# Kernel tuning notes

Hardware: AMD Instinct MI355X
Metric: run time of the kernel (lower is better)

Reference implementation:

```python
import jax, jax.numpy as jnp
import numpy as np

N, E = 50000, 800000
S, V, RBF_DIM = 128, 16, 16
RBF_DMAX = 20.0
MSG_NORM = 10.0
EPS = 1e-8
DVH_M = V + 1            # message GVP: dim_vectors_in = V + 1 (edge direction appended), dim_h = max(17,16) = 17
FIN_M = S + RBF_DIM      # message GVP scalar input = node scalars + rbf(dist)
DVH_U = 2 * V            # update GVP: dim_vectors_in = 2V (node + aggregated), dim_h = 32
FIN_U = 2 * S


def _rbf(D):
    # [E] -> [E, RBF_DIM], matches torch _rbf with D_min=0, D_max=20, D_count=16
    D_mu = jnp.linspace(0.0, RBF_DMAX, RBF_DIM)
    D_sigma = RBF_DMAX / RBF_DIM
    return jnp.exp(-(((D[:, None] - D_mu[None, :]) / D_sigma) ** 2))


def _gvp(s, v, Wh, Wu, Wf, bf, Wg, bg):
    # s: [n, F_in], v: [n, V_in, 3]; faithful to GVP.forward with sigmoid vector gating
    Vh = jnp.einsum('nvc,vh->nhc', v, Wh)          # [n, H, 3]
    Vu = jnp.einsum('nhc,ho->noc', Vh, Wu)         # [n, V_out, 3]
    sh = jnp.sqrt(jnp.clip(jnp.sum(Vh * Vh, -1), EPS))  # _norm_no_nan
    feats_out = jax.nn.silu(jnp.concatenate([s, sh], -1) @ Wf + bf)
    gate = jax.nn.sigmoid(feats_out @ Wg + bg)[..., None]
    return feats_out, gate * Vu


def _gvp_layernorm(s, v, gamma, beta):
    mu = jnp.mean(s, -1, keepdims=True)
    var = jnp.mean((s - mu) ** 2, -1, keepdims=True)
    s_out = (s - mu) / jnp.sqrt(var + 1e-5) * gamma + beta
    vn = jnp.clip(jnp.sum(v * v, -1, keepdims=True), EPS)        # [N, V, 1]
    vn = jnp.sqrt(jnp.mean(vn, -2, keepdims=True) + 1e-5) + 1e-5  # [N, 1, 1]
    return s_out, v / vn


def setup_inputs() -> dict:
    key = jax.random.key(0)
    ks = jax.random.split(key, 14)
    rn = lambda k, shp, sc: (jax.random.normal(k, shp, dtype=jnp.float32) * sc)
    inp = {
        's': rn(ks[0], (N, S), 1.0),
        'v': rn(ks[1], (N, V, 3), 1.0),
        'x': rn(ks[2], (N, 3), 5.0),
        # message GVP params
        'Wh_m': rn(ks[3], (DVH_M, DVH_M), 1.0 / np.sqrt(DVH_M)),
        'Wu_m': rn(ks[4], (DVH_M, V), 1.0 / np.sqrt(DVH_M)),
        'Wf_m': rn(ks[5], (DVH_M + FIN_M, S), 1.0 / np.sqrt(DVH_M + FIN_M)),
        'bf_m': jnp.zeros((S,), jnp.float32),
        'Wg_m': rn(ks[6], (S, V), 1.0 / np.sqrt(S)),
        'bg_m': jnp.zeros((V,), jnp.float32),
        # update GVP params
        'Wh_u': rn(ks[7], (DVH_U, DVH_U), 1.0 / np.sqrt(DVH_U)),
        'Wu_u': rn(ks[8], (DVH_U, V), 1.0 / np.sqrt(DVH_U)),
        'Wf_u': rn(ks[9], (DVH_U + FIN_U, S), 1.0 / np.sqrt(DVH_U + FIN_U)),
        'bf_u': jnp.zeros((S,), jnp.float32),
        'Wg_u': rn(ks[10], (S, V), 1.0 / np.sqrt(S)),
        'bg_u': jnp.zeros((V,), jnp.float32),
        # layernorm
        'ln_g': jnp.ones((S,), jnp.float32),
        'ln_b': jnp.zeros((S,), jnp.float32),
        'edge_index': jax.random.randint(ks[11], (2, E), 0, N),
    }
    return inp


def reference(s, v, x, Wh_m, Wu_m, Wf_m, bf_m, Wg_m, bg_m,
              Wh_u, Wu_u, Wf_u, bf_u, Wg_u, bg_u, ln_g, ln_b, edge_index):
    src, dst = edge_index[0], edge_index[1]
    # gather + geometric edge features
    dx = x[dst] - x[src]                                   # [E, 3]
    dist = jnp.sqrt(jnp.clip(jnp.sum(dx * dx, -1), EPS))    # [E]
    unit = dx / dist[:, None]
    v_in = jnp.concatenate([v[src], unit[:, None, :]], 1)   # [E, V+1, 3]
    s_in = jnp.concatenate([s[src], _rbf(dist)], -1)        # [E, S+RBF]
    # message GVP
    ms, mv = _gvp(s_in, v_in, Wh_m, Wu_m, Wf_m, bf_m, Wg_m, bg_m)
    # scatter-reduce + message norm
    agg_s = jax.ops.segment_sum(ms, dst, num_segments=N) / MSG_NORM   # [N, S]
    agg_v = jax.ops.segment_sum(mv, dst, num_segments=N) / MSG_NORM   # [N, V, 3]
    # update GVP on concatenated node + aggregated messages
    us, uv = _gvp(jnp.concatenate([s, agg_s], -1), jnp.concatenate([v, agg_v], 1),
                  Wh_u, Wu_u, Wf_u, bf_u, Wg_u, bg_u)
    # residual + GVPLayerNorm
    return _gvp_layernorm(s + us, v + uv, ln_g, ln_b)
```

## Files before the change

### kernel.cpp

```cpp
#include <hip/hip_runtime.h>
#include <hip/hip_bf16.h>
#include <math.h>

#define N_NODES 50000
#define E_EDGES 800000
#define S_DIM 128
#define V_DIM 16
#define HM 17
#define KM 161
#define HU 32
#define KU 288

#define EB 32
#define LDA 164
#define NB 32
#define LDA2 292

__device__ __forceinline__ float bf2f(unsigned short u) {
    union { unsigned int i; float f; } w; w.i = ((unsigned int)u) << 16; return w.f;
}
__device__ __forceinline__ unsigned short f2bf(float f) {
    union { float f; unsigned int i; } w; w.f = f;
    unsigned int x = w.i;
    x += 0x7fff + ((x >> 16) & 1);
    return (unsigned short)(x >> 16);
}
__device__ __forceinline__ float silu_f(float x) { return x / (1.f + __expf(-x)); }
__device__ __forceinline__ float sigm_f(float x) { return 1.f / (1.f + __expf(-x)); }
__device__ __forceinline__ float ldf(const void* p, int i, int m) {
    if (m) return ((const float*)p)[i];
    return bf2f(((const unsigned short*)p)[i]);
}

__global__ void detect_kernel(const unsigned short* __restrict__ s_us,
                              int* __restrict__ flag) {
    int t = threadIdx.x;
    int huge = 0;
    for (int k = 0; k < 16; ++k) {
        unsigned short u = s_us[2 * (t + 64 * k)];
        int e = (u >> 7) & 0xFF;
        if (e > 140) huge = 1;
    }
    if (huge) atomicOr(flag, 1);
}

__global__ void hist_kernel(const int* __restrict__ ei, int* __restrict__ cnt) {
    int i = blockIdx.x * 256 + threadIdx.x;
    if (i < E_EDGES) atomicAdd(&cnt[ei[E_EDGES + i]], 1);
}

__global__ void scan_kernel(int* __restrict__ cnt) {
    __shared__ int buf[1024];
    __shared__ int base_s;
    const int t = threadIdx.x;
    if (t == 0) base_s = 0;
    __syncthreads();
    for (int c0 = 0; c0 < N_NODES; c0 += 1024) {
        int i = c0 + t;
        int v = (i < N_NODES) ? cnt[i] : 0;
        buf[t] = v;
        __syncthreads();
        for (int off = 1; off < 1024; off <<= 1) {
            int tmp = (t >= off) ? buf[t - off] : 0;
            __syncthreads();
            buf[t] += tmp;
            __syncthreads();
        }
        int base = base_s;
        if (i < N_NODES) cnt[i] = base + buf[t] - v;
        __syncthreads();
        if (t == 0) base_s = base + buf[1023];
        __syncthreads();
    }
}

__global__ void scatter_kernel(const int* __restrict__ ei,
                               int* __restrict__ cnt,
                               int* __restrict__ perm) {
    int i = blockIdx.x * 256 + threadIdx.x;
    if (i < E_EDGES) {
        int d = ei[E_EDGES + i];
        int p = atomicAdd(&cnt[d], 1);
        perm[p] = i;
    }
}

__global__ __launch_bounds__(256, 4) void edge_kernel(
    const void* sP, const void* vP, const void* xP,
    const void* WhP, const void* WuP, const void* WfP,
    const void* bfP, const void* WgP, const void* bgP,
    const int* __restrict__ ei,
    const int* __restrict__ perm,
    const int* __restrict__ flagp,
    float* __restrict__ agg_s,
    float* __restrict__ agg_v)
{
    __shared__ float A[EB * LDA];
    __shared__ float Bs[2048];
    __shared__ float WhWu[HM * 16];
    __shared__ float gates[EB * 16];
    __shared__ int srcb[EB], dstb[EB];

    const int t = threadIdx.x;
    const int e0 = blockIdx.x * EB;
    const int m = flagp[0];

    if (t < EB) {
        int eid = perm[e0 + t];
        srcb[t] = ei[eid];
        dstb[t] = ei[E_EDGES + eid];
    }
    if (m) {
        const float* Wh = (const float*)WhP;
        const float* Wu = (const float*)WuP;
        for (int i = t; i < HM * HM; i += 256) gates[i] = Wh[i];
        for (int i = t; i < HM * 16; i += 256) Bs[1664 + i] = Wu[i];
    } else {
        const unsigned short* Wh = (const unsigned short*)WhP;
        const unsigned short* Wu = (const unsigned short*)WuP;
        for (int i = t; i < HM * HM; i += 256) gates[i] = bf2f(Wh[i]);
        for (int i = t; i < HM * 16; i += 256) Bs[1664 + i] = bf2f(Wu[i]);
    }
    __syncthreads();

    for (int idx = t; idx < HM * 16; idx += 256) {
        int vv = idx / 16, o = idx % 16;
        float acc = 0.f;
        for (int h = 0; h < HM; ++h)
            acc += gates[vv * HM + h] * Bs[1664 + h * 16 + o];
        WhWu[idx] = acc;
    }
    {
        int tj = t & 31, te = t >> 5;
        if (m) {
            const float* sF = (const float*)sP;
            for (int r = 0; r < 4; ++r) {
                int e = te + 8 * r;
                float4 u = *(const float4*)(sF + (size_t)srcb[e] * S_DIM + tj * 4);
                float* a = &A[e * LDA + tj * 4];
                a[0] = u.x; a[1] = u.y; a[2] = u.z; a[3] = u.w;
            }
        } else {
            const unsigned short* sU = (const unsigned short*)sP;
            for (int r = 0; r < 4; ++r) {
                int e = te + 8 * r;
                ushort4 u = *(const ushort4*)(sU + (size_t)srcb[e] * S_DIM + tj * 4);
                float* a = &A[e * LDA + tj * 4];
                a[0] = bf2f(u.x); a[1] = bf2f(u.y); a[2] = bf2f(u.z); a[3] = bf2f(u.w);
            }
        }
    }
    if (t < 128) {
        int e = t >> 2, q = t & 3;
        int src = srcb[e];
        float* vin = &Bs[e * 52 + q * 12];
        if (m) {
            const float* vp = (const float*)vP + (size_t)src * 48 + q * 12;
            for (int i = 0; i < 3; ++i) {
                float4 u = *(const float4*)(vp + i * 4);
                vin[i * 4 + 0] = u.x; vin[i * 4 + 1] = u.y;
                vin[i * 4 + 2] = u.z; vin[i * 4 + 3] = u.w;
            }
        } else {
            const unsigned short* vp = (const unsigned short*)vP + (size_t)src * 48 + q * 12;
            for (int i = 0; i < 3; ++i) {
                ushort4 u = *(const ushort4*)(vp + i * 4);
                vin[i * 4 + 0] = bf2f(u.x); vin[i * 4 + 1] = bf2f(u.y);
                vin[i * 4 + 2] = bf2f(u.z); vin[i * 4 + 3] = bf2f(u.w);
            }
        }
        if (q == 0) {
            int dst = dstb[e];
            float dxc[3]; float d2 = 0.f;
            for (int c = 0; c < 3; ++c) {
                float xs = ldf(xP, src * 3 + c, m);
                float xd = ldf(xP, dst * 3 + c, m);
                dxc[c] = xd - xs; d2 += dxc[c] * dxc[c];
            }
            float dist = sqrtf(fmaxf(d2, 1e-8f));
            float inv = 1.f / dist;
            for (int c = 0; c < 3; ++c) Bs[e * 52 + 48 + c] = dxc[c] * inv;
            for (int k = 0; k < 16; ++k) {
                float mu = (20.f / 15.f) * (float)k;
                float z = (dist - mu) * (1.f / 1.25f);
                A[e * LDA + 128 + k] = __expf(-z * z);
            }
        }
    }
    __syncthreads();

    for (int idx = t; idx < EB * HM; idx += 256) {
        int e = idx / HM, h = idx % HM;
        const float* vin = &Bs[e * 52];
        float vh0 = 0.f, vh1 = 0.f, vh2 = 0.f;
        for (int vv = 0; vv < HM; ++vv) {
            float w = gates[vv * HM + h];
            vh0 += vin[vv * 3 + 0] * w;
            vh1 += vin[vv * 3 + 1] * w;
            vh2 += vin[vv * 3 + 2] * w;
        }
        A[e * LDA + 144 + h] = sqrtf(fmaxf(vh0 * vh0 + vh1 * vh1 + vh2 * vh2, 1e-8f));
    }
    float vureg[6];
    for (int r = 0; r < 6; ++r) {
        int idx = t + 256 * r;
        int e = idx / 48, oc = idx % 48, o = oc / 3, c = oc % 3;
        const float* vin = &Bs[e * 52];
        float acc = 0.f;
        for (int vv = 0; vv < HM; ++vv)
            acc += vin[vv * 3 + c] * WhWu[vv * 16 + o];
        vureg[r] = acc;
    }
    __syncthreads();

    const int tj = t & 15, te = t >> 4;
    const int eb = te * 2;
    float acc[2][8];
    #pragma unroll
    for (int i = 0; i < 2; ++i)
        #pragma unroll
        for (int j = 0; j < 8; ++j) acc[i][j] = 0.f;

    for (int kk = 0; kk < KM; kk += 16) {
        int kmax = min(16, KM - kk);
        if (m) {
            const float* WfF = (const float*)WfP;
            for (int idx = t; idx < kmax * 32; idx += 256) {
                int kt = idx >> 5, col4 = (idx & 31) * 4;
                float4 u = *(const float4*)(WfF + (size_t)(kk + kt) * 128 + col4);
                float* b = &Bs[kt * 128 + col4];
                b[0] = u.x; b[1] = u.y; b[2] = u.z; b[3] = u.w;
            }
        } else {
            const unsigned short* WfU = (const unsigned short*)WfP;
            for (int idx = t; idx < kmax * 32; idx += 256) {
                int kt = idx >> 5, col4 = (idx & 31) * 4;
                ushort4 u = *(const ushort4*)(WfU + (size_t)(kk + kt) * 128 + col4);
                float* b = &Bs[kt * 128 + col4];
                b[0] = bf2f(u.x); b[1] = bf2f(u.y); b[2] = bf2f(u.z); b[3] = bf2f(u.w);
            }
        }
        __syncthreads();
        for (int kt = 0; kt < kmax; ++kt) {
            float a0 = A[(eb + 0) * LDA + kk + kt];
            float a1 = A[(eb + 1) * LDA + kk + kt];
            const float* brow = &Bs[kt * 128 + tj];
            #pragma unroll
            for (int jj = 0; jj < 8; ++jj) {
                float b = brow[16 * jj];
                acc[0][jj] += a0 * b; acc[1][jj] += a1 * b;
            }
        }
        __syncthreads();
    }
    float breg[8];
    #pragma unroll
    for (int jj = 0; jj < 8; ++jj) breg[jj] = ldf(bfP, tj + 16 * jj, m);
    #pragma unroll
    for (int i = 0; i < 2; ++i) {
        float* aout = &A[(eb + i) * LDA];
        #pragma unroll
        for (int jj = 0; jj < 8; ++jj)
            aout[tj + 16 * jj] = silu_f(acc[i][jj] + breg[jj]);
    }
    __syncthreads();
    if (m) {
        const float* Wg = (const float*)WgP;
        for (int i = t; i < 2048; i += 256) Bs[i] = Wg[i];
    } else {
        const unsigned short* Wg = (const unsigned short*)WgP;
        for (int i = t; i < 2048; i += 256) Bs[i] = bf2f(Wg[i]);
    }
    __syncthreads();
    for (int r = 0; r < 2; ++r) {
        int idx = t + 256 * r;
        int e = idx / 16, o = idx % 16;
        const float* fe = &A[e * LDA];
        float g = ldf(bgP, o, m);
        for (int j = 0; j < S_DIM; ++j)
            g += fe[j] * Bs[j * 16 + o];
        gates[idx] = sigm_f(g);
    }
    __syncthreads();
    for (int r = 0; r < 6; ++r) {
        int idx = t + 256 * r;
        int e = idx / 48, oc = idx % 48, o = oc / 3;
        (void)oc;
        Bs[idx] = vureg[r] * gates[e * 16 + o];
    }
    __syncthreads();
    if (t < 176) {
        float run = 0.f;
        int cur = dstb[0];
        if (t < 128) {
            const int col = t;
            for (int e = 0; e < EB; ++e) {
                int d = dstb[e];
                if (d != cur) {
                    atomicAdd(&agg_s[(size_t)cur * S_DIM + col], run);
                    run = 0.f; cur = d;
                }
                run += A[e * LDA + col];
            }
            atomicAdd(&agg_s[(size_t)cur * S_DIM + col], run);
        } else {
            const int oc = t - 128;
            for (int e = 0; e < EB; ++e) {
                int d = dstb[e];
                if (d != cur) {
                    atomicAdd(&agg_v[(size_t)cur * 48 + oc], run);
                    run = 0.f; cur = d;
                }
                run += Bs[e * 48 + oc];
            }
            atomicAdd(&agg_v[(size_t)cur * 48 + oc], run);
        }
    }
}

__global__ __launch_bounds__(256) void node_kernel(
    const void* sP, const void* vP,
    const void* WhP, const void* WuP, const void* WfP,
    const void* bfP, const void* WgP, const void* bgP,
    const void* lngP, const void* lnbP,
    const int* __restrict__ flagp,
    const float* __restrict__ agg_s,
    const float* __restrict__ agg_v,
    void* outP)
{
    __shared__ float A2[NB * LDA2];
    __shared__ float Bs2[4096];
    __shared__ float WhWu2[HU * 16];
    __shared__ float gates2[NB * 16];
    __shared__ float WhS[HU * HU];
    __shared__ float mu_s[NB], rstd_s[NB], vn_s[NB];

    const int t = threadIdx.x;
    const int n0 = blockIdx.x * NB;
    const int m = flagp[0];

    if (m) {
        const float* Wh = (const float*)WhP;
        const float* Wu = (const float*)WuP;
        for (int i = t; i < HU * HU; i += 256) WhS[i] = Wh[i];
        for (int i = t; i < HU * 16; i += 256) gates2[i] = Wu[i];
    } else {
        const unsigned short* Wh = (const unsigned short*)WhP;
        const unsigned short* Wu = (const unsigned short*)WuP;
        for (int i = t; i < HU * HU; i += 256) WhS[i] = bf2f(Wh[i]);
        for (int i = t; i < HU * 16; i += 256) gates2[i] = bf2f(Wu[i]);
    }
    if (m) {
        const float* sF = (const float*)sP;
        for (int idx = t; idx < NB * 32; idx += 256) {
            int ni = idx >> 5, col4 = (idx & 31) * 4;
            int n = n0 + ni;
            float* a = &A2[ni * LDA2 + col4];
            if (n < N_NODES) {
                float4 u = *(const float4*)(sF + (size_t)n * 128 + col4);
                a[0] = u.x; a[1] = u.y; a[2] = u.z; a[3] = u.w;
            } else { a[0] = a[1] = a[2] = a[3] = 0.f; }
        }
    } else {
        const unsigned short* sU = (const unsigned short*)sP;
        for (int idx = t; idx < NB * 32; idx += 256) {
            int ni = idx >> 5, col4 = (idx & 31) * 4;
            int n = n0 + ni;
            float* a = &A2[ni * LDA2 + col4];
            if (n < N_NODES) {
                ushort4 u = *(const ushort4*)(sU + (size_t)n * 128 + col4);
                a[0] = bf2f(u.x); a[1] = bf2f(u.y); a[2] = bf2f(u.z); a[3] = bf2f(u.w);
            } else { a[0] = a[1] = a[2] = a[3] = 0.f; }
        }
    }
    for (int idx = t; idx < NB * 32; idx += 256) {
        int ni = idx >> 5, col4 = (idx & 31) * 4;
        int n = n0 + ni;
        float* a = &A2[ni * LDA2 + 128 + col4];
        if (n < N_NODES) {
            float4 u = *(const float4*)(agg_s + (size_t)n * 128 + col4);
            a[0] = u.x * 0.1f; a[1] = u.y * 0.1f; a[2] = u.z * 0.1f; a[3] = u.w * 0.1f;
        } else { a[0] = a[1] = a[2] = a[3] = 0.f; }
    }
    for (int idx = t; idx < NB * 96; idx += 256) {
        int ni = idx / 96, vc = idx % 96;
        int n = n0 + ni;
        float val = 0.f;
        if (n < N_NODES)
            val = (vc < 48) ? ldf(vP, n * 48 + vc, m)
                            : agg_v[(size_t)n * 48 + (vc - 48)] * 0.1f;
        Bs2[ni * 100 + vc] = val;
    }
    __syncthreads();
    for (int idx = t; idx < HU * 16; idx += 256) {
        int vv = idx / 16, o = idx % 16;
        float acc = 0.f;
        for (int h = 0; h < HU; ++h)
            acc += WhS[vv * HU + h] * gates2[h * 16 + o];
        WhWu2[idx] = acc;
    }
    for (int idx = t; idx < NB * HU; idx += 256) {
        int ni = idx / HU, h = idx % HU;
        const float* vc = &Bs2[ni * 100];
        float vh0 = 0.f, vh1 = 0.f, vh2 = 0.f;
        for (int vv = 0; vv < HU; ++vv) {
            float w = WhS[vv * HU + h];
            vh0 += vc[vv * 3 + 0] * w; vh1 += vc[vv * 3 + 1] * w; vh2 += vc[vv * 3 + 2] * w;
        }
        A2[ni * LDA2 + 256 + h] = sqrtf(fmaxf(vh0 * vh0 + vh1 * vh1 + vh2 * vh2, 1e-8f));
    }
    __syncthreads();
    float vureg[6];
    for (int r = 0; r < 6; ++r) {
        int idx = t + 256 * r;
        int ni = idx / 48, oc = idx % 48, o = oc / 3, c = oc % 3;
        const float* vc = &Bs2[ni * 100];
        float acc = 0.f;
        for (int vv = 0; vv < HU; ++vv)
            acc += vc[vv * 3 + c] * WhWu2[vv * 16 + o];
        vureg[r] = acc;
    }
    __syncthreads();

    const int tj = t & 15, tn = t >> 4;
    const int nb = tn * 2;
    float acc[2][8];
    #pragma unroll
    for (int i = 0; i < 2; ++i)
        #pragma unroll
        for (int j = 0; j < 8; ++j) acc[i][j] = 0.f;

    for (int kk = 0; kk < KU; kk += 32) {
        if (m) {
            const float* WfF = (const float*)WfP;
            for (int idx = t; idx < 32 * 32; idx += 256) {
                int kt = idx >> 5, col4 = (idx & 31) * 4;
                float4 u = *(const float4*)(WfF + (size_t)(kk + kt) * 128 + col4);
                float* b = &Bs2[kt * 128 + col4];
                b[0] = u.x; b[1] = u.y; b[2] = u.z; b[3] = u.w;
            }
        } else {
            const unsigned short* WfU = (const unsigned short*)WfP;
            for (int idx = t; idx < 32 * 32; idx += 256) {
                int kt = idx >> 5, col4 = (idx & 31) * 4;
                ushort4 u = *(const ushort4*)(WfU + (size_t)(kk + kt) * 128 + col4);
                float* b = &Bs2[kt * 128 + col4];
                b[0] = bf2f(u.x); b[1] = bf2f(u.y); b[2] = bf2f(u.z); b[3] = bf2f(u.w);
            }
        }
        __syncthreads();
        for (int kt = 0; kt < 32; ++kt) {
            float a0 = A2[(nb + 0) * LDA2 + kk + kt];
            float a1 = A2[(nb + 1) * LDA2 + kk + kt];
            const float* brow = &Bs2[kt * 128 + tj];
            #pragma unroll
            for (int jj = 0; jj < 8; ++jj) {
                float b = brow[16 * jj];
                acc[0][jj] += a0 * b; acc[1][jj] += a1 * b;
            }
        }
        __syncthreads();
    }
    float breg[8];
    #pragma unroll
    for (int jj = 0; jj < 8; ++jj) breg[jj] = ldf(bfP, tj + 16 * jj, m);
    #pragma unroll
    for (int i = 0; i < 2; ++i) {
        float* aout = &A2[(nb + i) * LDA2 + 128];
        #pragma unroll
        for (int jj = 0; jj < 8; ++jj)
            aout[tj + 16 * jj] = silu_f(acc[i][jj] + breg[jj]);
    }
    __syncthreads();
    if (m) {
        const float* Wg = (const float*)WgP;
        for (int i = t; i < 2048; i += 256) Bs2[i] = Wg[i];
    } else {
        const unsigned short* Wg = (const unsigned short*)WgP;
        for (int i = t; i < 2048; i += 256) Bs2[i] = bf2f(Wg[i]);
    }
    __syncthreads();
    for (int r = 0; r < 2; ++r) {
        int idx = t + 256 * r;
        int ni = idx / 16, o = idx % 16;
        const float* fe = &A2[ni * LDA2 + 128];
        float g = ldf(bgP, o, m);
        for (int j = 0; j < 128; ++j)
            g += fe[j] * Bs2[j * 16 + o];
        gates2[idx] = sigm_f(g);
    }
    __syncthreads();
    for (int r = 0; r < 6; ++r) {
        int idx = t + 256 * r;
        int ni = idx / 48, oc = idx % 48, o = oc / 3;
        int n = n0 + ni;
        float vres = 0.f;
        if (n < N_NODES)
            vres = ldf(vP, n * 48 + oc, m) + vureg[r] * gates2[ni * 16 + o];
        Bs2[ni * 48 + oc] = vres;
    }
    __syncthreads();
    if (t < NB) {
        const float* arow = &A2[t * LDA2];
        float sum = 0.f, sumsq = 0.f;
        for (int j = 0; j < 128; ++j) {
            float xr = arow[j] + arow[128 + j];
            sum += xr; sumsq += xr * xr;
        }
        float mu = sum * (1.f / 128.f);
        float var = sumsq * (1.f / 128.f) - mu * mu;
        mu_s[t] = mu;
        rstd_s[t] = rsqrtf(fmaxf(var, 0.f) + 1e-5f);
        const float* vr = &Bs2[t * 48];
        float accv = 0.f;
        for (int o = 0; o < 16; ++o) {
            float mm = vr[o*3]*vr[o*3] + vr[o*3+1]*vr[o*3+1] + vr[o*3+2]*vr[o*3+2];
            accv += fmaxf(mm, 1e-8f);
        }
        vn_s[t] = sqrtf(accv * (1.f / 16.f) + 1e-5f) + 1e-5f;
    }
    __syncthreads();
    float* outF = (float*)outP;
    unsigned short* outU = (unsigned short*)outP;
    for (int idx = t; idx < NB * 128; idx += 256) {
        int ni = idx >> 7, j = idx & 127;
        int n = n0 + ni;
        if (n < N_NODES) {
            float xr = A2[ni * LDA2 + j] + A2[ni * LDA2 + 128 + j];
            float o = (xr - mu_s[ni]) * rstd_s[ni] * ldf(lngP, j, m) + ldf(lnbP, j, m);
            if (m) outF[(size_t)n * 128 + j] = o;
            else   outU[(size_t)n * 128 + j] = f2bf(o);
        }
    }
    for (int idx = t; idx < NB * 48; idx += 256) {
        int ni = idx / 48, oc = idx % 48;
        int n = n0 + ni;
        if (n < N_NODES) {
            float o = Bs2[ni * 48 + oc] / vn_s[ni];
            if (m) outF[(size_t)N_NODES * 128 + (size_t)n * 48 + oc] = o;
            else   outU[(size_t)N_NODES * 128 + (size_t)n * 48 + oc] = f2bf(o);
        }
    }
}

extern "C" void kernel_launch(void* const* d_in, const int* in_sizes, int n_in,
                              void* d_out, int out_size, void* d_ws, size_t ws_size,
                              hipStream_t stream) {
    const int* ei = (const int*)d_in[17];

    int* flag = (int*)d_ws;
    int* cnt = (int*)((char*)d_ws + 64);
    float* agg_s = (float*)((char*)d_ws + 64 + 200000);
    float* agg_v = agg_s + (size_t)N_NODES * 128;
    int* perm = (int*)(agg_v + (size_t)N_NODES * 48);

    hipMemsetAsync(d_ws, 0,
                   64 + 200000 + (size_t)N_NODES * (128 + 48) * sizeof(float),
                   stream);

    detect_kernel<<<1, 64, 0, stream>>>((const unsigned short*)d_in[0], flag);

    hist_kernel<<<(E_EDGES + 255) / 256, 256, 0, stream>>>(ei, cnt);
    scan_kernel<<<1, 1024, 0, stream>>>(cnt);
    scatter_kernel<<<(E_EDGES + 255) / 256, 256, 0, stream>>>(ei, cnt, perm);

    edge_kernel<<<E_EDGES / EB, 256, 0, stream>>>(
        d_in[0], d_in[1], d_in[2], d_in[3], d_in[4], d_in[5],
        d_in[6], d_in[7], d_in[8], ei, perm, flag, agg_s, agg_v);
    node_kernel<<<(N_NODES + NB - 1) / NB, 256, 0, stream>>>(
        d_in[0], d_in[1], d_in[9], d_in[10], d_in[11], d_in[12],
        d_in[13], d_in[14], d_in[15], d_in[16], flag,
        agg_s, agg_v, d_out);
}
```

Before: 2.534 ms.

## Make edge kernel persistent over tiles with Wf and Wg cached in LDS

Each edge block now processes eight 32-edge tiles. In the bf16 path it loads the whole Wf and Wg weights into shared memory once, as bf16, instead of restaging Wf through LDS in chunks for every tile. The scatter pass now writes sorted src/dst arrays directly, which removes the indirection through perm. The trade-offs are more LDS use (launch bounds drop to 2 blocks per CU), fewer blocks, and an fp32 path that reads Wg straight from global memory.

```diff
diff --git a/kernel.cpp b/kernel.cpp
--- a/kernel.cpp
+++ b/kernel.cpp
@@ -12,6 +12,7 @@
 #define KU 288
 
 #define EB 32
+#define TILES 8
 #define LDA 164
 #define NB 32
 #define LDA2 292
@@ -76,50 +77,55 @@
 
 __global__ void scatter_kernel(const int* __restrict__ ei,
                                int* __restrict__ cnt,
-                               int* __restrict__ perm) {
+                               int* __restrict__ src_sorted,
+                               int* __restrict__ dst_sorted) {
     int i = blockIdx.x * 256 + threadIdx.x;
     if (i < E_EDGES) {
         int d = ei[E_EDGES + i];
         int p = atomicAdd(&cnt[d], 1);
-        perm[p] = i;
-    }
-}
-
-__global__ __launch_bounds__(256, 4) void edge_kernel(
+        src_sorted[p] = ei[i];
+        dst_sorted[p] = d;
+    }
+}
+
+__global__ __launch_bounds__(256, 2) void edge_kernel(
     const void* sP, const void* vP, const void* xP,
     const void* WhP, const void* WuP, const void* WfP,
     const void* bfP, const void* WgP, const void* bgP,
-    const int* __restrict__ ei,
-    const int* __restrict__ perm,
+    const int* __restrict__ src_sorted,
+    const int* __restrict__ dst_sorted,
     const int* __restrict__ flagp,
     float* __restrict__ agg_s,
     float* __restrict__ agg_v)
 {
+    __shared__ __align__(16) unsigned short WfU[KM * 128];
+    __shared__ __align__(16) unsigned short WgU[128 * 16];
     __shared__ float A[EB * LDA];
     __shared__ float Bs[2048];
+    __shared__ float WhS[HM * HM];
     __shared__ float WhWu[HM * 16];
     __shared__ float gates[EB * 16];
     __shared__ int srcb[EB], dstb[EB];
 
     const int t = threadIdx.x;
-    const int e0 = blockIdx.x * EB;
     const int m = flagp[0];
 
-    if (t < EB) {
-        int eid = perm[e0 + t];
-        srcb[t] = ei[eid];
-        dstb[t] = ei[E_EDGES + eid];
-    }
     if (m) {
         const float* Wh = (const float*)WhP;
         const float* Wu = (const float*)WuP;
-        for (int i = t; i < HM * HM; i += 256) gates[i] = Wh[i];
+        for (int i = t; i < HM * HM; i += 256) WhS[i] = Wh[i];
         for (int i = t; i < HM * 16; i += 256) Bs[1664 + i] = Wu[i];
     } else {
         const unsigned short* Wh = (const unsigned short*)WhP;
         const unsigned short* Wu = (const unsigned short*)WuP;
-        for (int i = t; i < HM * HM; i += 256) gates[i] = bf2f(Wh[i]);
+        for (int i = t; i < HM * HM; i += 256) WhS[i] = bf2f(Wh[i]);
         for (int i = t; i < HM * 16; i += 256) Bs[1664 + i] = bf2f(Wu[i]);
+        const ushort4* Wf4 = (const ushort4*)WfP;
+        ushort4* WfD = (ushort4*)WfU;
+        for (int i = t; i < (KM * 128) / 4; i += 256) WfD[i] = Wf4[i];
+        const ushort4* Wg4 = (const ushort4*)WgP;
+        ushort4* WgD = (ushort4*)WgU;
+        for (int i = t; i < (128 * 16) / 4; i += 256) WgD[i] = Wg4[i];
     }
     __syncthreads();
 
@@ -127,194 +133,217 @@
         int vv = idx / 16, o = idx % 16;
         float acc = 0.f;
         for (int h = 0; h < HM; ++h)
-            acc += gates[vv * HM + h] * Bs[1664 + h * 16 + o];
+            acc += WhS[vv * HM + h] * Bs[1664 + h * 16 + o];
         WhWu[idx] = acc;
     }
-    {
-        int tj = t & 31, te = t >> 5;
-        if (m) {
-            const float* sF = (const float*)sP;
-            for (int r = 0; r < 4; ++r) {
-                int e = te + 8 * r;
-                float4 u = *(const float4*)(sF + (size_t)srcb[e] * S_DIM + tj * 4);
-                float* a = &A[e * LDA + tj * 4];
-                a[0] = u.x; a[1] = u.y; a[2] = u.z; a[3] = u.w;
-            }
-        } else {
-            const unsigned short* sU = (const unsigned short*)sP;
-            for (int r = 0; r < 4; ++r) {
-                int e = te + 8 * r;
-                ushort4 u = *(const ushort4*)(sU + (size_t)srcb[e] * S_DIM + tj * 4);
-                float* a = &A[e * LDA + tj * 4];
-                a[0] = bf2f(u.x); a[1] = bf2f(u.y); a[2] = bf2f(u.z); a[3] = bf2f(u.w);
-            }
-        }
-    }
-    if (t < 128) {
-        int e = t >> 2, q = t & 3;
-        int src = srcb[e];
-        float* vin = &Bs[e * 52 + q * 12];
-        if (m) {
-            const float* vp = (const float*)vP + (size_t)src * 48 + q * 12;
-            for (int i = 0; i < 3; ++i) {
-                float4 u = *(const float4*)(vp + i * 4);
-                vin[i * 4 + 0] = u.x; vin[i * 4 + 1] = u.y;
-                vin[i * 4 + 2] = u.z; vin[i * 4 + 3] = u.w;
-            }
-        } else {
-            const unsigned short* vp = (const unsigned short*)vP + (size_t)src * 48 + q * 12;
-            for (int i = 0; i < 3; ++i) {
-                ushort4 u = *(const ushort4*)(vp + i * 4);
-                vin[i * 4 + 0] = bf2f(u.x); vin[i * 4 + 1] = bf2f(u.y);
-                vin[i * 4 + 2] = bf2f(u.z); vin[i * 4 + 3] = bf2f(u.w);
-            }
-        }
-        if (q == 0) {
-            int dst = dstb[e];
-            float dxc[3]; float d2 = 0.f;
-            for (int c = 0; c < 3; ++c) {
-                float xs = ldf(xP, src * 3 + c, m);
-                float xd = ldf(xP, dst * 3 + c, m);
-                dxc[c] = xd - xs; d2 += dxc[c] * dxc[c];
-            }
-            float dist = sqrtf(fmaxf(d2, 1e-8f));
-            float inv = 1.f / dist;
-            for (int c = 0; c < 3; ++c) Bs[e * 52 + 48 + c] = dxc[c] * inv;
-            for (int k = 0; k < 16; ++k) {
-                float mu = (20.f / 15.f) * (float)k;
-                float z = (dist - mu) * (1.f / 1.25f);
-                A[e * LDA + 128 + k] = __expf(-z * z);
-            }
-        }
-    }
-    __syncthreads();
-
-    for (int idx = t; idx < EB * HM; idx += 256) {
-        int e = idx / HM, h = idx % HM;
-        const float* vin = &Bs[e * 52];
-        float vh0 = 0.f, vh1 = 0.f, vh2 = 0.f;
-        for (int vv = 0; vv < HM; ++vv) {
-            float w = gates[vv * HM + h];
-            vh0 += vin[vv * 3 + 0] * w;
-            vh1 += vin[vv * 3 + 1] * w;
-            vh2 += vin[vv * 3 + 2] * w;
-        }
-        A[e * LDA + 144 + h] = sqrtf(fmaxf(vh0 * vh0 + vh1 * vh1 + vh2 * vh2, 1e-8f));
-    }
-    float vureg[6];
-    for (int r = 0; r < 6; ++r) {
-        int idx = t + 256 * r;
-        int e = idx / 48, oc = idx % 48, o = oc / 3, c = oc % 3;
-        const float* vin = &Bs[e * 52];
-        float acc = 0.f;
-        for (int vv = 0; vv < HM; ++vv)
-            acc += vin[vv * 3 + c] * WhWu[vv * 16 + o];
-        vureg[r] = acc;
-    }
-    __syncthreads();
 
     const int tj = t & 15, te = t >> 4;
     const int eb = te * 2;
-    float acc[2][8];
-    #pragma unroll
-    for (int i = 0; i < 2; ++i)
-        #pragma unroll
-        for (int j = 0; j < 8; ++j) acc[i][j] = 0.f;
-
-    for (int kk = 0; kk < KM; kk += 16) {
-        int kmax = min(16, KM - kk);
-        if (m) {
-            const float* WfF = (const float*)WfP;
-            for (int idx = t; idx < kmax * 32; idx += 256) {
-                int kt = idx >> 5, col4 = (idx & 31) * 4;
-                float4 u = *(const float4*)(WfF + (size_t)(kk + kt) * 128 + col4);
-                float* b = &Bs[kt * 128 + col4];
-                b[0] = u.x; b[1] = u.y; b[2] = u.z; b[3] = u.w;
-            }
-        } else {
-            const unsigned short* WfU = (const unsigned short*)WfP;
-            for (int idx = t; idx < kmax * 32; idx += 256) {
-                int kt = idx >> 5, col4 = (idx & 31) * 4;
-                ushort4 u = *(const ushort4*)(WfU + (size_t)(kk + kt) * 128 + col4);
-                float* b = &Bs[kt * 128 + col4];
-                b[0] = bf2f(u.x); b[1] = bf2f(u.y); b[2] = bf2f(u.z); b[3] = bf2f(u.w);
-            }
-        }
-        __syncthreads();
-        for (int kt = 0; kt < kmax; ++kt) {
-            float a0 = A[(eb + 0) * LDA + kk + kt];
-            float a1 = A[(eb + 1) * LDA + kk + kt];
-            const float* brow = &Bs[kt * 128 + tj];
-            #pragma unroll
-            for (int jj = 0; jj < 8; ++jj) {
-                float b = brow[16 * jj];
-                acc[0][jj] += a0 * b; acc[1][jj] += a1 * b;
-            }
-        }
-        __syncthreads();
-    }
     float breg[8];
     #pragma unroll
-    for (int jj = 0; jj < 8; ++jj) breg[jj] = ldf(bfP, tj + 16 * jj, m);
-    #pragma unroll
-    for (int i = 0; i < 2; ++i) {
-        float* aout = &A[(eb + i) * LDA];
+    for (int jj = 0; jj < 8; ++jj) breg[jj] = ldf(bfP, tj * 8 + jj, m);
+    __syncthreads();
+
+    for (int tile = 0; tile < TILES; ++tile) {
+        const int e0 = blockIdx.x * (EB * TILES) + tile * EB;
+
+        if (t < EB) {
+            srcb[t] = src_sorted[e0 + t];
+            dstb[t] = dst_sorted[e0 + t];
+        }
+        __syncthreads();
+
+        {
+            int cj = t & 31, ce = t >> 5;
+            if (m) {
+                const float* sF = (const float*)sP;
+                for (int r = 0; r < 4; ++r) {
+                    int e = ce + 8 * r;
+                    float4 u = *(const float4*)(sF + (size_t)srcb[e] * S_DIM + cj * 4);
+                    float* a = &A[e * LDA + cj * 4];
+                    a[0] = u.x; a[1] = u.y; a[2] = u.z; a[3] = u.w;
+                }
+            } else {
+                const unsigned short* sU = (const unsigned short*)sP;
+                for (int r = 0; r < 4; ++r) {
+                    int e = ce + 8 * r;
+                    ushort4 u = *(const ushort4*)(sU + (size_t)srcb[e] * S_DIM + cj * 4);
+                    float* a = &A[e * LDA + cj * 4];
+                    a[0] = bf2f(u.x); a[1] = bf2f(u.y); a[2] = bf2f(u.z); a[3] = bf2f(u.w);
+                }
+            }
+        }
+        if (t < 128) {
+            int e = t >> 2, q = t & 3;
+            int src = srcb[e];
+            float* vin = &Bs[e * 52 + q * 12];
+            if (m) {
+                const float* vp = (const float*)vP + (size_t)src * 48 + q * 12;
+                for (int i = 0; i < 3; ++i) {
+                    float4 u = *(const float4*)(vp + i * 4);
+                    vin[i * 4 + 0] = u.x; vin[i * 4 + 1] = u.y;
+                    vin[i * 4 + 2] = u.z; vin[i * 4 + 3] = u.w;
+                }
+            } else {
+                const unsigned short* vp = (const unsigned short*)vP + (size_t)src * 48 + q * 12;
+                for (int i = 0; i < 3; ++i) {
+                    ushort4 u = *(const ushort4*)(vp + i * 4);
+                    vin[i * 4 + 0] = bf2f(u.x); vin[i * 4 + 1] = bf2f(u.y);
+                    vin[i * 4 + 2] = bf2f(u.z); vin[i * 4 + 3] = bf2f(u.w);
+                }
+            }
+            if (q == 0) {
+                int dst = dstb[e];
+                float dxc[3]; float d2 = 0.f;
+                for (int c = 0; c < 3; ++c) {
+                    float xs = ldf(xP, src * 3 + c, m);
+                    float xd = ldf(xP, dst * 3 + c, m);
+                    dxc[c] = xd - xs; d2 += dxc[c] * dxc[c];
+                }
+                float dist = sqrtf(fmaxf(d2, 1e-8f));
+                float inv = 1.f / dist;
+                for (int c = 0; c < 3; ++c) Bs[e * 52 + 48 + c] = dxc[c] * inv;
+                for (int k = 0; k < 16; ++k) {
+                    float mu = (20.f / 15.f) * (float)k;
+                    float z = (dist - mu) * (1.f / 1.25f);
+                    A[e * LDA + 128 + k] = __expf(-z * z);
+                }
+            }
+        }
+        __syncthreads();
+
+        for (int idx = t; idx < EB * HM; idx += 256) {
+            int e = idx / HM, h = idx % HM;
+            const float* vin = &Bs[e * 52];
+            float vh0 = 0.f, vh1 = 0.f, vh2 = 0.f;
+            for (int vv = 0; vv < HM; ++vv) {
+                float w = WhS[vv * HM + h];
+                vh0 += vin[vv * 3 + 0] * w;
+                vh1 += vin[vv * 3 + 1] * w;
+                vh2 += vin[vv * 3 + 2] * w;
+            }
+            A[e * LDA + 144 + h] = sqrtf(fmaxf(vh0 * vh0 + vh1 * vh1 + vh2 * vh2, 1e-8f));
+        }
+        float vureg[6];
+        for (int r = 0; r < 6; ++r) {
+            int idx = t + 256 * r;
+            int e = idx / 48, oc = idx % 48, o = oc / 3, c = oc % 3;
+            const float* vin = &Bs[e * 52];
+            float acc = 0.f;
+            for (int vv = 0; vv < HM; ++vv)
+                acc += vin[vv * 3 + c] * WhWu[vv * 16 + o];
+            vureg[r] = acc;
+        }
+        __syncthreads();
+
+        float acc[2][8];
         #pragma unroll
-        for (int jj = 0; jj < 8; ++jj)
-            aout[tj + 16 * jj] = silu_f(acc[i][jj] + breg[jj]);
-    }
-    __syncthreads();
-    if (m) {
-        const float* Wg = (const float*)WgP;
-        for (int i = t; i < 2048; i += 256) Bs[i] = Wg[i];
-    } else {
-        const unsigned short* Wg = (const unsigned short*)WgP;
-        for (int i = t; i < 2048; i += 256) Bs[i] = bf2f(Wg[i]);
-    }
-    __syncthreads();
-    for (int r = 0; r < 2; ++r) {
-        int idx = t + 256 * r;
-        int e = idx / 16, o = idx % 16;
-        const float* fe = &A[e * LDA];
-        float g = ldf(bgP, o, m);
-        for (int j = 0; j < S_DIM; ++j)
-            g += fe[j] * Bs[j * 16 + o];
-        gates[idx] = sigm_f(g);
-    }
-    __syncthreads();
-    for (int r = 0; r < 6; ++r) {
-        int idx = t + 256 * r;
-        int e = idx / 48, oc = idx % 48, o = oc / 3;
-        (void)oc;
-        Bs[idx] = vureg[r] * gates[e * 16 + o];
-    }
-    __syncthreads();
-    if (t < 176) {
-        float run = 0.f;
-        int cur = dstb[0];
-        if (t < 128) {
-            const int col = t;
-            for (int e = 0; e < EB; ++e) {
-                int d = dstb[e];
-                if (d != cur) {
-                    atomicAdd(&agg_s[(size_t)cur * S_DIM + col], run);
-                    run = 0.f; cur = d;
-                }
-                run += A[e * LDA + col];
-            }
-            atomicAdd(&agg_s[(size_t)cur * S_DIM + col], run);
+        for (int i = 0; i < 2; ++i)
+            #pragma unroll
+            for (int j = 0; j < 8; ++j) acc[i][j] = 0.f;
+
+        if (m) {
+            for (int kk = 0; kk < KM; kk += 16) {
+                int kmax = min(16, KM - kk);
+                const float* WfF = (const float*)WfP;
+                for (int idx = t; idx < kmax * 32; idx += 256) {
+                    int kt = idx >> 5, col4 = (idx & 31) * 4;
+                    float4 u = *(const float4*)(WfF + (size_t)(kk + kt) * 128 + col4);
+                    float* b = &Bs[kt * 128 + col4];
+                    b[0] = u.x; b[1] = u.y; b[2] = u.z; b[3] = u.w;
+                }
+                __syncthreads();
+                for (int kt = 0; kt < kmax; ++kt) {
+                    float a0 = A[(eb + 0) * LDA + kk + kt];
+                    float a1 = A[(eb + 1) * LDA + kk + kt];
+                    const float* brow = &Bs[kt * 128 + tj * 8];
+                    #pragma unroll
+                    for (int jj = 0; jj < 8; ++jj) {
+                        float b = brow[jj];
+                        acc[0][jj] += a0 * b; acc[1][jj] += a1 * b;
+                    }
+                }
+                __syncthreads();
+            }
         } else {
-            const int oc = t - 128;
-            for (int e = 0; e < EB; ++e) {
-                int d = dstb[e];
-                if (d != cur) {
-                    atomicAdd(&agg_v[(size_t)cur * 48 + oc], run);
-                    run = 0.f; cur = d;
-                }
-                run += Bs[e * 48 + oc];
-            }
-            atomicAdd(&agg_v[(size_t)cur * 48 + oc], run);
-        }
+            for (int kt = 0; kt < KM; ++kt) {
+                float a0 = A[(eb + 0) * LDA + kt];
+                float a1 = A[(eb + 1) * LDA + kt];
+                const ushort4* wrow = (const ushort4*)&WfU[kt * 128 + tj * 8];
+                ushort4 w0 = wrow[0], w1 = wrow[1];
+                float b0 = bf2f(w0.x), b1 = bf2f(w0.y), b2 = bf2f(w0.z), b3 = bf2f(w0.w);
+                float b4 = bf2f(w1.x), b5 = bf2f(w1.y), b6 = bf2f(w1.z), b7 = bf2f(w1.w);
+                acc[0][0] += a0 * b0; acc[1][0] += a1 * b0;
+                acc[0][1] += a0 * b1; acc[1][1] += a1 * b1;
+                acc[0][2] += a0 * b2; acc[1][2] += a1 * b2;
+                acc[0][3] += a0 * b3; acc[1][3] += a1 * b3;
+                acc[0][4] += a0 * b4; acc[1][4] += a1 * b4;
+                acc[0][5] += a0 * b5; acc[1][5] += a1 * b5;
+                acc[0][6] += a0 * b6; acc[1][6] += a1 * b6;
+                acc[0][7] += a0 * b7; acc[1][7] += a1 * b7;
+            }
+            __syncthreads();
+        }
+
+        #pragma unroll
+        for (int i = 0; i < 2; ++i) {
+            float* aout = &A[(eb + i) * LDA + tj * 8];
+            #pragma unroll
+            for (int jj = 0; jj < 8; ++jj)
+                aout[jj] = silu_f(acc[i][jj] + breg[jj]);
+        }
+        __syncthreads();
+
+        for (int r = 0; r < 2; ++r) {
+            int idx = t + 256 * r;
+            int e = idx / 16, o = idx % 16;
+            const float* fe = &A[e * LDA];
+            float g = ldf(bgP, o, m);
+            if (m) {
+                const float* Wg = (const float*)WgP;
+                for (int j = 0; j < S_DIM; ++j)
+                    g += fe[j] * Wg[j * 16 + o];
+            } else {
+                for (int j = 0; j < S_DIM; ++j)
+                    g += fe[j] * bf2f(WgU[j * 16 + o]);
+            }
+            gates[idx] = sigm_f(g);
+        }
+        __syncthreads();
+        for (int r = 0; r < 6; ++r) {
+            int idx = t + 256 * r;
+            int e = idx / 48, o = (idx % 48) / 3;
+            Bs[idx] = vureg[r] * gates[e * 16 + o];
+        }
+        __syncthreads();
+        if (t < 176) {
+            float run = 0.f;
+            int cur = dstb[0];
+            if (t < 128) {
+                const int col = t;
+                for (int e = 0; e < EB; ++e) {
+                    int d = dstb[e];
+                    if (d != cur) {
+                        atomicAdd(&agg_s[(size_t)cur * S_DIM + col], run);
+                        run = 0.f; cur = d;
+                    }
+                    run += A[e * LDA + col];
+                }
+                atomicAdd(&agg_s[(size_t)cur * S_DIM + col], run);
+            } else {
+                const int oc = t - 128;
+                for (int e = 0; e < EB; ++e) {
+                    int d = dstb[e];
+                    if (d != cur) {
+                        atomicAdd(&agg_v[(size_t)cur * 48 + oc], run);
+                        run = 0.f; cur = d;
+                    }
+                    run += Bs[e * 48 + oc];
+                }
+                atomicAdd(&agg_v[(size_t)cur * 48 + oc], run);
+            }
+        }
+        __syncthreads();
     }
 }
 
@@ -440,10 +469,10 @@
                 b[0] = u.x; b[1] = u.y; b[2] = u.z; b[3] = u.w;
             }
         } else {
-            const unsigned short* WfU = (const unsigned short*)WfP;
+            const unsigned short* WfU2 = (const unsigned short*)WfP;
             for (int idx = t; idx < 32 * 32; idx += 256) {
                 int kt = idx >> 5, col4 = (idx & 31) * 4;
-                ushort4 u = *(const ushort4*)(WfU + (size_t)(kk + kt) * 128 + col4);
+                ushort4 u = *(const ushort4*)(WfU2 + (size_t)(kk + kt) * 128 + col4);
                 float* b = &Bs2[kt * 128 + col4];
                 b[0] = bf2f(u.x); b[1] = bf2f(u.y); b[2] = bf2f(u.z); b[3] = bf2f(u.w);
             }
@@ -550,23 +579,24 @@
 
     int* flag = (int*)d_ws;
     int* cnt = (int*)((char*)d_ws + 64);
-    float* agg_s = (float*)((char*)d_ws + 64 + 200000);
+    int* src_sorted = (int*)((char*)d_ws + 64 + 200000);
+    int* dst_sorted = src_sorted + E_EDGES;
+    float* agg_s = (float*)(dst_sorted + E_EDGES);
     float* agg_v = agg_s + (size_t)N_NODES * 128;
-    int* perm = (int*)(agg_v + (size_t)N_NODES * 48);
-
-    hipMemsetAsync(d_ws, 0,
-                   64 + 200000 + (size_t)N_NODES * (128 + 48) * sizeof(float),
-                   stream);
+
+    size_t zbytes = 64 + 200000 + (size_t)E_EDGES * 2 * sizeof(int)
+                  + (size_t)N_NODES * (128 + 48) * sizeof(float);
+    hipMemsetAsync(d_ws, 0, zbytes, stream);
 
     detect_kernel<<<1, 64, 0, stream>>>((const unsigned short*)d_in[0], flag);
 
     hist_kernel<<<(E_EDGES + 255) / 256, 256, 0, stream>>>(ei, cnt);
     scan_kernel<<<1, 1024, 0, stream>>>(cnt);
-    scatter_kernel<<<(E_EDGES + 255) / 256, 256, 0, stream>>>(ei, cnt, perm);
-
-    edge_kernel<<<E_EDGES / EB, 256, 0, stream>>>(
+    scatter_kernel<<<(E_EDGES + 255) / 256, 256, 0, stream>>>(ei, cnt, src_sorted, dst_sorted);
+
+    edge_kernel<<<E_EDGES / (EB * TILES), 256, 0, stream>>>(
         d_in[0], d_in[1], d_in[2], d_in[3], d_in[4], d_in[5],
-        d_in[6], d_in[7], d_in[8], ei, perm, flag, agg_s, agg_v);
+        d_in[6], d_in[7], d_in[8], src_sorted, dst_sorted, flag, agg_s, agg_v);
     node_kernel<<<(N_NODES + NB - 1) / NB, 256, 0, stream>>>(
         d_in[0], d_in[1], d_in[9], d_in[10], d_in[11], d_in[12],
         d_in[13], d_in[14], d_in[15], d_in[16], flag,
```

After: 3.847 ms. 51.8% more time.
